# Kernel tuning notes

Hardware: AMD Instinct MI355X
Metric: run time of the kernel (lower is better)

## Reference

```python
import jax, jax.numpy as jnp
import numpy as np

H = 1024  # hidden_size
V = 32000  # vocab_size
L = 2048  # y_len


def _lstm_cell(gates, c):
    # torch gate order: input, forget, cell(g), output
    i = jax.nn.sigmoid(gates[:H])
    f = jax.nn.sigmoid(gates[H:2 * H])
    g = jnp.tanh(gates[2 * H:3 * H])
    o = jax.nn.sigmoid(gates[3 * H:4 * H])
    c_new = f * c + i * g
    return o * jnp.tanh(c_new), c_new


def setup_inputs() -> dict:
    key = jax.random.key(0)
    ks = jax.random.split(key, 13)
    s = 0.05
    inp = {
        "y": jax.random.randint(ks[0], (L,), 0, V, dtype=jnp.int32),
        "context_vector": jax.random.normal(ks[1], (2, H), dtype=jnp.float32),
        # layer 0: input dim 1
        "w_ih0": jax.random.normal(ks[2], (4 * H, 1), dtype=jnp.float32) * s,
        "w_hh0": jax.random.normal(ks[3], (4 * H, H), dtype=jnp.float32) * s,
        "b_ih0": jax.random.normal(ks[4], (4 * H,), dtype=jnp.float32) * s,
        "b_hh0": jax.random.normal(ks[5], (4 * H,), dtype=jnp.float32) * s,
        # layer 1: input dim H
        "w_ih1": jax.random.normal(ks[6], (4 * H, H), dtype=jnp.float32) * s,
        "w_hh1": jax.random.normal(ks[7], (4 * H, H), dtype=jnp.float32) * s,
        "b_ih1": jax.random.normal(ks[8], (4 * H,), dtype=jnp.float32) * s,
        "b_hh1": jax.random.normal(ks[9], (4 * H,), dtype=jnp.float32) * s,
        # fc: hidden -> vocab
        "w_fc": jax.random.normal(ks[10], (V, H), dtype=jnp.float32) * s,
        "b_fc": jax.random.normal(ks[11], (V,), dtype=jnp.float32) * s,
    }
    return inp


def reference(y, context_vector, w_ih0, w_hh0, b_ih0, b_hh0,
              w_ih1, w_hh1, b_ih1, b_hh1, w_fc, b_fc):
    # tfr = 0.0 => teacher forcing never used; next input is argmax of predictions.
    # h_s = h_c = context_vector initially (as in the torch module).
    def step(carry, _):
        tok, h, c = carry  # tok: scalar f32; h,c: [2, H]
        x = tok[None]  # [1]
        g0 = w_ih0 @ x + b_ih0 + w_hh0 @ h[0] + b_hh0
        h0, c0 = _lstm_cell(g0, c[0])
        g1 = w_ih1 @ h0 + b_ih1 + w_hh1 @ h[1] + b_hh1
        h1, c1 = _lstm_cell(g1, c[1])
        preds = jax.nn.relu(w_fc @ h1 + b_fc)  # [V]
        best = jnp.argmax(preds).astype(jnp.float32)
        return (best, jnp.stack([h0, h1]), jnp.stack([c0, c1])), preds

    init = (y[0].astype(jnp.float32), context_vector, context_vector)
    _, preds_seq = jax.lax.scan(step, init, None, length=L - 1)  # [L-1, V]
    outputs = jnp.concatenate(
        [jnp.zeros((1, V), dtype=jnp.float32), preds_seq], axis=0)  # [L, V]
    return outputs  # training mode: raw outputs (eval would apply log_softmax)
```

## Files before the change

kernel.cpp:

```cpp
#include <hip/hip_runtime.h>
#include <cstdint>
#include <cstddef>

#define H   1024
#define V   32000
#define L   2048
#define G4  4096
#define NB  256
#define NT  1024
#define RPB (V / NB)

#define GNB   500
#define GT    512
#define GS    8
#define GR    8
#define NCHUNK (L / GS)

__device__ __forceinline__ float wave_reduce_sum(float v) {
    #pragma unroll
    for (int off = 32; off > 0; off >>= 1) v += __shfl_down(v, off);
    return v;
}

__device__ __forceinline__ float wave_reduce_max(float v) {
    #pragma unroll
    for (int off = 32; off > 0; off >>= 1) v = fmaxf(v, __shfl_down(v, off));
    return v;
}

__device__ __forceinline__ unsigned long long wave_reduce_max_u64(unsigned long long v) {
    #pragma unroll
    for (int off = 32; off > 0; off >>= 1) {
        const unsigned long long o = __shfl_down(v, off);
        v = (o > v) ? o : v;
    }
    return v;
}

__device__ __forceinline__ float sigmoidf_(float x) {
    return 1.0f / (1.0f + expf(-x));
}

__device__ __forceinline__ float dot4(const float4 w, const float* __restrict__ h, int c) {
    return w.x * h[c] + w.y * h[c + 1] + w.z * h[c + 2] + w.w * h[c + 3];
}

__device__ __forceinline__ float sb2f(int w, int pos) {
    return (float)((w << ((3 - pos) * 8)) >> 24);
}

__global__ __launch_bounds__(256) void quant_fc(
    const float* __restrict__ src, signed char* __restrict__ dst,
    float2* __restrict__ scl_eps)
{
    const int gw   = (blockIdx.x * blockDim.x + threadIdx.x) >> 6;
    const int lane = threadIdx.x & 63;
    const int nw   = (gridDim.x * blockDim.x) >> 6;
    for (int row = gw; row < V; row += nw) {
        const float* p = src + (size_t)row * H + lane * 16;
        float w[16];
        #pragma unroll
        for (int j = 0; j < 4; j++) {
            const float4 f = *(const float4*)(p + j * 4);
            w[j * 4 + 0] = f.x; w[j * 4 + 1] = f.y;
            w[j * 4 + 2] = f.z; w[j * 4 + 3] = f.w;
        }
        float m = 0.f;
        #pragma unroll
        for (int j = 0; j < 16; j++) m = fmaxf(m, fabsf(w[j]));
        m = wave_reduce_max(m);
        m = __shfl(m, 0);
        const float scale = fmaxf(m, 1e-30f) / 127.f;
        const float inv   = 127.f / fmaxf(m, 1e-30f);
        int q[16];
        float esq = 0.f;
        #pragma unroll
        for (int j = 0; j < 16; j++) {
            q[j] = __float2int_rn(w[j] * inv);
            const float e = w[j] - scale * (float)q[j];
            esq += e * e;
        }
        esq = wave_reduce_sum(esq);
        const unsigned int d0 = (q[0] & 255) | ((q[1] & 255) << 8) | ((q[2] & 255) << 16) | ((unsigned int)(q[3] & 255) << 24);
        const unsigned int d1 = (q[4] & 255) | ((q[5] & 255) << 8) | ((q[6] & 255) << 16) | ((unsigned int)(q[7] & 255) << 24);
        const unsigned int d2 = (q[8] & 255) | ((q[9] & 255) << 8) | ((q[10] & 255) << 16) | ((unsigned int)(q[11] & 255) << 24);
        const unsigned int d3 = (q[12] & 255) | ((q[13] & 255) << 8) | ((q[14] & 255) << 16) | ((unsigned int)(q[15] & 255) << 24);
        *(int4*)(dst + (size_t)row * H + lane * 16) =
            make_int4((int)d0, (int)d1, (int)d2, (int)d3);
        if (lane == 0) {
            scl_eps[row] = make_float2(scale, sqrtf(esq) + 1e-12f);
        }
    }
}

__global__ __launch_bounds__(NT) void init_kernel(
    const int* __restrict__ y, const float* __restrict__ ctx,
    const float* __restrict__ w_hh0, const float* __restrict__ b_ih0,
    const float* __restrict__ b_hh0,
    float* __restrict__ v0, float* __restrict__ c0, float* __restrict__ c1,
    float* __restrict__ h1g0, unsigned long long* __restrict__ keys)
{
    __shared__ __align__(16) float h0s[H];
    const int b = blockIdx.x, t = threadIdx.x;
    h0s[t] = ctx[t];
    __syncthreads();

    const int wave = t >> 6, lane = t & 63;
    const int rowR = (wave >> 2) * H + b * 4 + (wave & 3);
    {
        const float* w0r = w_hh0 + (size_t)rowR * H;
        float accV = 0.f;
        #pragma unroll
        for (int k = 0; k < 4; k++) {
            const int c = k * 256 + lane * 4;
            accV += dot4(*(const float4*)(w0r + c), h0s, c);
        }
        accV = wave_reduce_sum(accV);
        if (lane == 0) v0[rowR] = accV + b_ih0[rowR] + b_hh0[rowR];
    }
    if (b == 0) {
        c0[t]   = ctx[t];
        c1[t]   = ctx[H + t];
        h1g0[t] = ctx[H + t];
        if (t < NB) keys[t] = 0ull;
        if (t == 0) {
            keys[0] = ((unsigned long long)0x7F800000u << 32) |
                      (0xFFFFFFFFu - (unsigned int)y[0]);
        }
    }
}

__global__ __launch_bounds__(NT) void lstm_kernel(
    const float* __restrict__ w_ih0, const float* __restrict__ w_ih1,
    const float* __restrict__ w_hh0, const float* __restrict__ w_hh1,
    const float* __restrict__ b_ih0, const float* __restrict__ b_hh0,
    const float* __restrict__ b_ih1, const float* __restrict__ b_hh1,
    const float* __restrict__ v0_in, float* __restrict__ v0_out,
    const float* __restrict__ c0_in, float* __restrict__ c0_out,
    float* __restrict__ c1,
    const float* __restrict__ h1prev, float* __restrict__ h1out,
    const unsigned long long* __restrict__ keys,
    float* __restrict__ h1_hist, const int step)
{
    __shared__ __align__(16) float h0s[H];
    __shared__ __align__(16) float h1ps[H];
    __shared__ float g1s[16];
    __shared__ unsigned long long kred[4];
    const int b = blockIdx.x, t = threadIdx.x;
    const int wave = t >> 6, lane = t & 63;
    const int rowR = (wave >> 2) * H + b * 4 + (wave & 3);

    const float* wU = w_hh1 + (size_t)rowR * H;
    float4 wu[4];
    #pragma unroll
    for (int k = 0; k < 4; k++)
        wu[k] = *(const float4*)(wU + k * 256 + lane * 4);

    h1ps[t] = h1prev[t];

    if (wave < 4) {
        unsigned long long k = keys[t];
        k = wave_reduce_max_u64(k);
        if (lane == 0) kred[wave] = k;
    }

    const float v0a = v0_in[t],         v0b = v0_in[H + t];
    const float v0c = v0_in[2 * H + t], v0d = v0_in[3 * H + t];
    const float wia = w_ih0[t],         wib = w_ih0[H + t];
    const float wic = w_ih0[2 * H + t], wid = w_ih0[3 * H + t];
    const float c0v = c0_in[t];

    __syncthreads();

    unsigned long long kk = kred[0];
    kk = (kred[1] > kk) ? kred[1] : kk;
    kk = (kred[2] > kk) ? kred[2] : kk;
    kk = (kred[3] > kk) ? kred[3] : kk;
    const float tok =
        (float)(unsigned int)(0xFFFFFFFFu - (unsigned int)(kk & 0xFFFFFFFFull));

    float accU = 0.f;
    #pragma unroll
    for (int k = 0; k < 4; k++) {
        const int c = k * 256 + lane * 4;
        accU += dot4(wu[k], h1ps, c);
    }

    {
        const float gi = v0a + tok * wia;
        const float gf = v0b + tok * wib;
        const float gg = v0c + tok * wic;
        const float go = v0d + tok * wid;
        const float i_ = sigmoidf_(gi);
        const float f_ = sigmoidf_(gf);
        const float g_ = tanhf(gg);
        const float o_ = sigmoidf_(go);
        const float cn = f_ * c0v + i_ * g_;
        if (b == 0) c0_out[t] = cn;
        h0s[t] = o_ * tanhf(cn);
    }
    __syncthreads();

    {
        const float* wA = w_ih1 + (size_t)rowR * H;
        const float* wB = w_hh0 + (size_t)rowR * H;
        float accA = 0.f, accB = 0.f;
        #pragma unroll
        for (int k = 0; k < 4; k++) {
            const int c = k * 256 + lane * 4;
            accA += dot4(*(const float4*)(wA + c), h0s, c);
            accB += dot4(*(const float4*)(wB + c), h0s, c);
        }
        const float g  = wave_reduce_sum(accA + accU);
        const float vv = wave_reduce_sum(accB);
        if (lane == 0) {
            g1s[wave]    = g  + b_ih1[rowR] + b_hh1[rowR];
            v0_out[rowR] = vv + b_ih0[rowR] + b_hh0[rowR];
        }
    }
    __syncthreads();

    if (t < 4) {
        const float i_ = sigmoidf_(g1s[t]);
        const float f_ = sigmoidf_(g1s[4 + t]);
        const float g_ = tanhf(g1s[8 + t]);
        const float o_ = sigmoidf_(g1s[12 + t]);
        const float cn = f_ * c1[b * 4 + t] + i_ * g_;
        c1[b * 4 + t] = cn;
        const float hv = o_ * tanhf(cn);
        h1out[b * 4 + t] = hv;
        if (h1_hist) h1_hist[(size_t)step * H + b * 4 + t] = hv;
    }
}

__global__ __launch_bounds__(NT) void screen_kernel(
    const signed char* __restrict__ wq8, const float2* __restrict__ scl_eps,
    const float* __restrict__ w_fc, const float* __restrict__ b_fc,
    const float* __restrict__ h1cur, unsigned long long* __restrict__ keys)
{
    __shared__ __align__(16) float h1s[H];
    __shared__ float lb[128], ub[128];
    __shared__ float red[16];
    __shared__ float LBmax_s;
    __shared__ unsigned long long wkey[16];
    const int b = blockIdx.x, t = threadIdx.x;
    const int wave = t >> 6, lane = t & 63;

    const float hv = h1cur[t];
    h1s[t] = hv;
    if (t < 128) { lb[t] = -3e38f; ub[t] = -3e38f; }
    {
        const float sq = wave_reduce_sum(hv * hv);
        if (lane == 0) red[wave] = sq;
    }
    __syncthreads();

    float Hl2;
    {
        float s = 0.f;
        #pragma unroll
        for (int i = 0; i < 16; i++) s += red[i];
        Hl2 = sqrtf(s);
    }

    const float4 hA = *(const float4*)(h1s + lane * 16);
    const float4 hB = *(const float4*)(h1s + lane * 16 + 4);
    const float4 hC = *(const float4*)(h1s + lane * 16 + 8);
    const float4 hD = *(const float4*)(h1s + lane * 16 + 12);

    int4 qv[8];
    #pragma unroll
    for (int i = 0; i < 8; i++) {
        const int rl = i * 16 + wave;
        const int row = b * RPB + (rl < RPB ? rl : 0);
        qv[i] = *(const int4*)(wq8 + (size_t)row * H + lane * 16);
    }
    float acc[8];
    #pragma unroll
    for (int i = 0; i < 8; i++) {
        const int4 q = qv[i];
        float a;
        a  = sb2f(q.x, 0) * hA.x + sb2f(q.x, 1) * hA.y + sb2f(q.x, 2) * hA.z + sb2f(q.x, 3) * hA.w;
        a += sb2f(q.y, 0) * hB.x + sb2f(q.y, 1) * hB.y + sb2f(q.y, 2) * hB.z + sb2f(q.y, 3) * hB.w;
        a += sb2f(q.z, 0) * hC.x + sb2f(q.z, 1) * hC.y + sb2f(q.z, 2) * hC.z + sb2f(q.z, 3) * hC.w;
        a += sb2f(q.w, 0) * hD.x + sb2f(q.w, 1) * hD.y + sb2f(q.w, 2) * hD.z + sb2f(q.w, 3) * hD.w;
        acc[i] = a;
    }
    #pragma unroll
    for (int off = 32; off > 0; off >>= 1) {
        #pragma unroll
        for (int i = 0; i < 8; i++) acc[i] += __shfl_down(acc[i], off);
    }
    if (lane == 0) {
        #pragma unroll
        for (int i = 0; i < 8; i++) {
            const int rl = i * 16 + wave;
            if (rl < RPB) {
                const int row = b * RPB + rl;
                const float2 se = scl_eps[row];
                float p = se.x * acc[i] + b_fc[row];
                p = fmaxf(p, 0.f);
                const float e = se.y * Hl2;
                ub[rl] = p + e;
                lb[rl] = p - e;
            }
        }
    }
    __syncthreads();

    if (wave == 0) {
        float m = fmaxf(lb[lane], lb[lane + 64]);
        m = wave_reduce_max(m);
        if (lane == 0) LBmax_s = m;
    }
    __syncthreads();
    const float LBmax = LBmax_s;

    unsigned long long bestKey = 0ull;

    #pragma unroll
    for (int i = 0; i < 8; i++) {
        const int rl = i * 16 + wave;
        if (rl >= RPB) break;
        if (ub[rl] >= LBmax) {
            const int row = b * RPB + rl;
            const float* wrow = w_fc + (size_t)row * H;
            float a = 0.f;
            #pragma unroll
            for (int k = 0; k < 4; k++) {
                const int c = k * 256 + lane * 4;
                a += dot4(*(const float4*)(wrow + c), h1s, c);
            }
            a = wave_reduce_sum(a);
            if (lane == 0) {
                float p = a + b_fc[row];
                p = p > 0.f ? p : 0.f;
                const unsigned long long key =
                    ((unsigned long long)__float_as_uint(p) << 32) |
                    (0xFFFFFFFFu - (unsigned int)row);
                if (key > bestKey) bestKey = key;
            }
        }
    }

    if (lane == 0) wkey[wave] = bestKey;
    __syncthreads();
    if (t == 0) {
        unsigned long long k = wkey[0];
        #pragma unroll
        for (int i = 1; i < 16; i++) k = (wkey[i] > k) ? wkey[i] : k;
        keys[b] = k;
    }
}

__global__ __launch_bounds__(NT) void fc32_kernel(
    const float* __restrict__ w_fc, const float* __restrict__ b_fc,
    const float* __restrict__ h1cur, unsigned long long* __restrict__ keys,
    float* __restrict__ out_row)
{
    __shared__ __align__(16) float h1s[H];
    __shared__ unsigned long long wkey[16];
    const int b = blockIdx.x, t = threadIdx.x;
    const int wave = t >> 6, lane = t & 63;

    h1s[t] = h1cur[t];
    __syncthreads();

    unsigned long long bestKey = 0ull;
    #pragma unroll
    for (int i = 0; i < 8; i++) {
        const int rl = i * 16 + wave;
        if (rl >= RPB) break;
        const int row = b * RPB + rl;
        const float* wrow = w_fc + (size_t)row * H;
        float a = 0.f;
        #pragma unroll
        for (int k = 0; k < 4; k++) {
            const int c = k * 256 + lane * 4;
            a += dot4(*(const float4*)(wrow + c), h1s, c);
        }
        a = wave_reduce_sum(a);
        if (lane == 0) {
            float p = a + b_fc[row];
            p = p > 0.f ? p : 0.f;
            out_row[row] = p;
            const unsigned long long key =
                ((unsigned long long)__float_as_uint(p) << 32) |
                (0xFFFFFFFFu - (unsigned int)row);
            if (key > bestKey) bestKey = key;
        }
    }

    if (lane == 0) wkey[wave] = bestKey;
    __syncthreads();
    if (t == 0) {
        unsigned long long k = wkey[0];
        #pragma unroll
        for (int i = 1; i < 16; i++) k = (wkey[i] > k) ? wkey[i] : k;
        keys[b] = k;
    }
}

__global__ __launch_bounds__(GT) void out_gemm(
    const float* __restrict__ w_fc, const float* __restrict__ b_fc,
    const float* __restrict__ h1_hist, float* __restrict__ out)
{
    __shared__ __align__(16) float hs[GS][H];
    __shared__ float stage[GS][64];
    const int b = blockIdx.x, t = threadIdx.x;
    const int wave = t >> 6, lane = t & 63;
    const int row0 = b * 64 + wave * GR;

    float4 wr[GR][4];
    #pragma unroll
    for (int r = 0; r < GR; r++)
        #pragma unroll
        for (int k = 0; k < 4; k++)
            wr[r][k] = *(const float4*)(w_fc + (size_t)(row0 + r) * H + k * 256 + lane * 4);

    for (int chunk = 0; chunk < NCHUNK; ++chunk) {
        __syncthreads();
        {
            const float4* src = (const float4*)(h1_hist + (size_t)chunk * GS * H);
            float4* dsts = (float4*)(&hs[0][0]);
            #pragma unroll
            for (int j = 0; j < 4; j++) dsts[j * GT + t] = src[j * GT + t];
        }
        __syncthreads();

        #pragma unroll
        for (int sb = 0; sb < 2; sb++) {
            float acc[GR][4];
            #pragma unroll
            for (int r = 0; r < GR; r++)
                #pragma unroll
                for (int s = 0; s < 4; s++) acc[r][s] = 0.f;
            #pragma unroll
            for (int k = 0; k < 4; k++) {
                const int c = k * 256 + lane * 4;
                const float4 h0 = *(const float4*)(&hs[sb * 4 + 0][c]);
                const float4 h1 = *(const float4*)(&hs[sb * 4 + 1][c]);
                const float4 h2 = *(const float4*)(&hs[sb * 4 + 2][c]);
                const float4 h3 = *(const float4*)(&hs[sb * 4 + 3][c]);
                #pragma unroll
                for (int r = 0; r < GR; r++) {
                    const float4 w = wr[r][k];
                    acc[r][0] += w.x * h0.x + w.y * h0.y + w.z * h0.z + w.w * h0.w;
                    acc[r][1] += w.x * h1.x + w.y * h1.y + w.z * h1.z + w.w * h1.w;
                    acc[r][2] += w.x * h2.x + w.y * h2.y + w.z * h2.z + w.w * h2.w;
                    acc[r][3] += w.x * h3.x + w.y * h3.y + w.z * h3.z + w.w * h3.w;
                }
            }
            #pragma unroll
            for (int r = 0; r < GR; r++)
                #pragma unroll
                for (int s = 0; s < 4; s++) {
                    const float vv = wave_reduce_sum(acc[r][s]);
                    if (lane == 0) stage[sb * 4 + s][wave * GR + r] = vv;
                }
        }
        __syncthreads();
        {
            const int s = t >> 6;
            const int col = t & 63;
            const int sidx = chunk * GS + s;
            if (sidx >= 1) {
                const float vv = stage[s][col] + b_fc[b * 64 + col];
                out[(size_t)sidx * V + b * 64 + col] = fmaxf(vv, 0.f);
            }
        }
    }
}

extern "C" void kernel_launch(void* const* d_in, const int* in_sizes, int n_in,
                              void* d_out, int out_size, void* d_ws, size_t ws_size,
                              hipStream_t stream)
{
    const int*   y     = (const int*)  d_in[0];
    const float* ctx   = (const float*)d_in[1];
    const float* w_ih0 = (const float*)d_in[2];
    const float* w_hh0 = (const float*)d_in[3];
    const float* b_ih0 = (const float*)d_in[4];
    const float* b_hh0 = (const float*)d_in[5];
    const float* w_ih1 = (const float*)d_in[6];
    const float* w_hh1 = (const float*)d_in[7];
    const float* b_ih1 = (const float*)d_in[8];
    const float* b_hh1 = (const float*)d_in[9];
    const float* w_fc  = (const float*)d_in[10];
    const float* b_fc  = (const float*)d_in[11];
    float* out = (float*)d_out;

    const size_t WQ8_BYTES  = (size_t)V * H;
    const size_t SCL_BYTES  = (size_t)V * sizeof(float2);
    const size_t HIST_BYTES = (size_t)L * H * sizeof(float);
    const size_t STATE_BYTES = 55296;
    const int use8 = (ws_size >= WQ8_BYTES + SCL_BYTES + HIST_BYTES + STATE_BYTES) ? 1 : 0;

    char* ws = (char*)d_ws;
    signed char* wq8     = (signed char*)ws;
    float2*      scl_eps = (float2*)(ws + WQ8_BYTES);
    float*       h1_hist = (float*)(ws + WQ8_BYTES + SCL_BYTES);
    char* base = ws + (use8 ? (WQ8_BYTES + SCL_BYTES + HIST_BYTES) : 0);
    float* v0g = (float*)(base + 0);
    float* c0  = (float*)(base + 32768);
    float* c1  = (float*)(base + 40960);
    float* h1g = (float*)(base + 45056);
    unsigned long long* keys = (unsigned long long*)(base + 53248);

    hipMemsetAsync(d_out, 0, (size_t)V * sizeof(float), stream);

    if (use8) {
        hipMemsetAsync(h1_hist, 0, (size_t)H * sizeof(float), stream);
        quant_fc<<<512, 256, 0, stream>>>(w_fc, wq8, scl_eps);
    }

    init_kernel<<<NB, NT, 0, stream>>>(y, ctx, w_hh0, b_ih0, b_hh0,
                                       v0g, c0, c1, h1g , keys);

    for (int t = 1; t < L; t++) {
        const float* v0i = v0g + ((t - 1) & 1) * G4;
        float*       v0o = v0g + (t & 1) * G4;
        const float* c0i = c0 + ((t - 1) & 1) * H;
        float*       c0o = c0 + (t & 1) * H;
        const float* h1p = h1g + ((t - 1) & 1) * H;
        float*       h1c = h1g + (t & 1) * H;
        lstm_kernel<<<NB, NT, 0, stream>>>(w_ih0, w_ih1, w_hh0, w_hh1,
                                           b_ih0, b_hh0, b_ih1, b_hh1,
                                           v0i, v0o, c0i, c0o, c1,
                                           h1p, h1c, keys,
                                           use8 ? h1_hist : (float*)nullptr, t);
        if (use8) {
            screen_kernel<<<NB, NT, 0, stream>>>(wq8, scl_eps, w_fc, b_fc,
                                                 h1c, keys);
        } else {
            fc32_kernel<<<NB, NT, 0, stream>>>(w_fc, b_fc, h1c, keys,
                                               out + (size_t)t * V);
        }
    }

    if (use8) {
        out_gemm<<<GNB, GT, 0, stream>>>(w_fc, b_fc, h1_hist, out);
    }
}
```

Before: 53.54 ms.

## Fuse per-step LSTM and screening kernels into one persistent kernel with grid barriers

Replaces roughly 4094 per-step kernel launches (lstm + screen) with a single persistent kernel of 256 blocks that loops over all time steps. Blocks synchronise through an atomic-counter grid barrier, and per-step state (h1, v0, argmax keys) moves through agent-scope atomic loads and stores. Weight slices for w_hh1, w_ih1 and w_hh0 stay in registers across steps, and the recurrent w_hh1·h1 product is computed early, overlapping the screen phase. This risks deadlock if all 256 blocks of 1024 threads cannot be co-resident, and it adds barrier spin latency in place of launch overhead.

```diff
diff --git a/kernel.cpp b/kernel.cpp
--- a/kernel.cpp
+++ b/kernel.cpp
@@ -47,6 +47,29 @@
 
 __device__ __forceinline__ float sb2f(int w, int pos) {
     return (float)((w << ((3 - pos) * 8)) >> 24);
+}
+
+__device__ __forceinline__ float ldc(const float* p) {
+    return __hip_atomic_load(p, __ATOMIC_RELAXED, __HIP_MEMORY_SCOPE_AGENT);
+}
+__device__ __forceinline__ void stc(float* p, float v) {
+    __hip_atomic_store(p, v, __ATOMIC_RELAXED, __HIP_MEMORY_SCOPE_AGENT);
+}
+__device__ __forceinline__ unsigned long long ldc64(const unsigned long long* p) {
+    return __hip_atomic_load(p, __ATOMIC_RELAXED, __HIP_MEMORY_SCOPE_AGENT);
+}
+__device__ __forceinline__ void stc64(unsigned long long* p, unsigned long long v) {
+    __hip_atomic_store(p, v, __ATOMIC_RELAXED, __HIP_MEMORY_SCOPE_AGENT);
+}
+
+__device__ __forceinline__ void gbar(unsigned int* cnt, unsigned int target) {
+    __syncthreads();
+    if (threadIdx.x == 0) {
+        __hip_atomic_fetch_add(cnt, 1u, __ATOMIC_RELAXED, __HIP_MEMORY_SCOPE_AGENT);
+        while (__hip_atomic_load(cnt, __ATOMIC_RELAXED, __HIP_MEMORY_SCOPE_AGENT) < target)
+            __builtin_amdgcn_s_sleep(4);
+    }
+    __syncthreads();
 }
 
 __global__ __launch_bounds__(256) void quant_fc(
@@ -93,6 +116,248 @@
     }
 }
 
+__global__ __launch_bounds__(NT) void persistent_kernel(
+    const int* __restrict__ y, const float* __restrict__ ctx,
+    const float* __restrict__ w_ih0, const float* __restrict__ w_ih1,
+    const float* __restrict__ w_hh0, const float* __restrict__ w_hh1,
+    const float* __restrict__ b_ih0, const float* __restrict__ b_hh0,
+    const float* __restrict__ b_ih1, const float* __restrict__ b_hh1,
+    const signed char* __restrict__ wq8, const float2* __restrict__ scl_eps,
+    const float* __restrict__ w_fc, const float* __restrict__ b_fc,
+    float* __restrict__ v0g, float* __restrict__ h1g,
+    unsigned long long* __restrict__ keys, unsigned int* __restrict__ cnt,
+    float* __restrict__ h1_hist)
+{
+    __shared__ __align__(16) float h0s[H];
+    __shared__ __align__(16) float hcs[H];
+    __shared__ float g1s[16];
+    __shared__ unsigned long long kred[4];
+    __shared__ float lb[128], ub[128];
+    __shared__ float red[16];
+    __shared__ float LBmax_s;
+    __shared__ unsigned long long wkey[16];
+    __shared__ float c1s[4];
+
+    const int b = blockIdx.x, t = threadIdx.x;
+    const int wave = t >> 6, lane = t & 63;
+    const int rowR = (wave >> 2) * H + b * 4 + (wave & 3);
+
+    unsigned int barK = 0;
+
+    float4 wu[4], wa[4], wb[4];
+    #pragma unroll
+    for (int k = 0; k < 4; k++) {
+        const int c = k * 256 + lane * 4;
+        wu[k] = *(const float4*)(w_hh1 + (size_t)rowR * H + c);
+        wa[k] = *(const float4*)(w_ih1 + (size_t)rowR * H + c);
+        wb[k] = *(const float4*)(w_hh0 + (size_t)rowR * H + c);
+    }
+    const float wia = w_ih0[t],         wib = w_ih0[H + t];
+    const float wic = w_ih0[2 * H + t], wid = w_ih0[3 * H + t];
+    const float bias0 = b_ih0[rowR] + b_hh0[rowR];
+    const float bias1 = b_ih1[rowR] + b_hh1[rowR];
+    float c0_reg = ctx[t];
+
+    h0s[t] = ctx[t];
+    hcs[t] = ctx[H + t];
+    if (t < 4) c1s[t] = ctx[H + b * 4 + t];
+    __syncthreads();
+    {
+        float accV = 0.f;
+        #pragma unroll
+        for (int k = 0; k < 4; k++) accV += dot4(wb[k], h0s, k * 256 + lane * 4);
+        accV = wave_reduce_sum(accV);
+        if (lane == 0) stc(&v0g[rowR], accV + bias0);
+    }
+    float accU = 0.f;
+    #pragma unroll
+    for (int k = 0; k < 4; k++) accU += dot4(wu[k], hcs, k * 256 + lane * 4);
+    if (b == 0 && t < NB) {
+        const unsigned long long seed =
+            ((unsigned long long)0x7F800000u << 32) |
+            (0xFFFFFFFFu - (unsigned int)y[0]);
+        stc64(&keys[t], (t == 0) ? seed : 0ull);
+    }
+    gbar(cnt, NB * (++barK));
+
+    for (int step = 1; step < L; ++step) {
+        const float* v0i = v0g + ((step - 1) & 1) * G4;
+        float*       v0o = v0g + (step & 1) * G4;
+        float*       h1c = h1g + (step & 1) * H;
+
+        if (wave < 4) {
+            unsigned long long k = ldc64(&keys[t]);
+            k = wave_reduce_max_u64(k);
+            if (lane == 0) kred[wave] = k;
+        }
+        const float v0a = ldc(&v0i[t]);
+        const float v0b = ldc(&v0i[H + t]);
+        const float v0c = ldc(&v0i[2 * H + t]);
+        const float v0d = ldc(&v0i[3 * H + t]);
+        __syncthreads();
+
+        unsigned long long kk = kred[0];
+        kk = (kred[1] > kk) ? kred[1] : kk;
+        kk = (kred[2] > kk) ? kred[2] : kk;
+        kk = (kred[3] > kk) ? kred[3] : kk;
+        const float tok =
+            (float)(unsigned int)(0xFFFFFFFFu - (unsigned int)(kk & 0xFFFFFFFFull));
+
+        {
+            const float gi = v0a + tok * wia;
+            const float gf = v0b + tok * wib;
+            const float gg = v0c + tok * wic;
+            const float go = v0d + tok * wid;
+            const float i_ = sigmoidf_(gi);
+            const float f_ = sigmoidf_(gf);
+            const float g_ = tanhf(gg);
+            const float o_ = sigmoidf_(go);
+            const float cn = f_ * c0_reg + i_ * g_;
+            c0_reg = cn;
+            h0s[t] = o_ * tanhf(cn);
+        }
+        __syncthreads();
+
+        {
+            float accA = 0.f, accB = 0.f;
+            #pragma unroll
+            for (int k = 0; k < 4; k++) {
+                const int c = k * 256 + lane * 4;
+                accA += dot4(wa[k], h0s, c);
+                accB += dot4(wb[k], h0s, c);
+            }
+            const float g  = wave_reduce_sum(accA + accU);
+            const float vv = wave_reduce_sum(accB);
+            if (lane == 0) {
+                g1s[wave] = g + bias1;
+                stc(&v0o[rowR], vv + bias0);
+            }
+        }
+        __syncthreads();
+
+        if (t < 4) {
+            const float i_ = sigmoidf_(g1s[t]);
+            const float f_ = sigmoidf_(g1s[4 + t]);
+            const float g_ = tanhf(g1s[8 + t]);
+            const float o_ = sigmoidf_(g1s[12 + t]);
+            const float cn = f_ * c1s[t] + i_ * g_;
+            c1s[t] = cn;
+            const float hv = o_ * tanhf(cn);
+            stc(&h1c[b * 4 + t], hv);
+            h1_hist[(size_t)step * H + b * 4 + t] = hv;
+        }
+        gbar(cnt, NB * (++barK));
+
+        if (t < 128) { lb[t] = -3e38f; ub[t] = -3e38f; }
+        const float hv2 = ldc(&h1c[t]);
+        hcs[t] = hv2;
+        {
+            const float sq = wave_reduce_sum(hv2 * hv2);
+            if (lane == 0) red[wave] = sq;
+        }
+        __syncthreads();
+
+        float s = 0.f;
+        #pragma unroll
+        for (int i = 0; i < 16; i++) s += red[i];
+        const float Hl2 = sqrtf(s);
+
+        const float4 hA = *(const float4*)(hcs + lane * 16);
+        const float4 hB = *(const float4*)(hcs + lane * 16 + 4);
+        const float4 hC = *(const float4*)(hcs + lane * 16 + 8);
+        const float4 hD = *(const float4*)(hcs + lane * 16 + 12);
+
+        float accs[8];
+        #pragma unroll
+        for (int bq = 0; bq < 2; bq++) {
+            int4 qv[4];
+            #pragma unroll
+            for (int i = 0; i < 4; i++) {
+                const int rl = (bq * 4 + i) * 16 + wave;
+                const int row = b * RPB + (rl < RPB ? rl : 0);
+                qv[i] = *(const int4*)(wq8 + (size_t)row * H + lane * 16);
+            }
+            #pragma unroll
+            for (int i = 0; i < 4; i++) {
+                const int4 q = qv[i];
+                float a;
+                a  = sb2f(q.x, 0) * hA.x + sb2f(q.x, 1) * hA.y + sb2f(q.x, 2) * hA.z + sb2f(q.x, 3) * hA.w;
+                a += sb2f(q.y, 0) * hB.x + sb2f(q.y, 1) * hB.y + sb2f(q.y, 2) * hB.z + sb2f(q.y, 3) * hB.w;
+                a += sb2f(q.z, 0) * hC.x + sb2f(q.z, 1) * hC.y + sb2f(q.z, 2) * hC.z + sb2f(q.z, 3) * hC.w;
+                a += sb2f(q.w, 0) * hD.x + sb2f(q.w, 1) * hD.y + sb2f(q.w, 2) * hD.z + sb2f(q.w, 3) * hD.w;
+                accs[bq * 4 + i] = a;
+            }
+        }
+        #pragma unroll
+        for (int off = 32; off > 0; off >>= 1) {
+            #pragma unroll
+            for (int i = 0; i < 8; i++) accs[i] += __shfl_down(accs[i], off);
+        }
+        if (lane == 0) {
+            #pragma unroll
+            for (int i = 0; i < 8; i++) {
+                const int rl = i * 16 + wave;
+                if (rl < RPB) {
+                    const int row = b * RPB + rl;
+                    const float2 se = scl_eps[row];
+                    float p = se.x * accs[i] + b_fc[row];
+                    p = fmaxf(p, 0.f);
+                    const float e = se.y * Hl2;
+                    ub[rl] = p + e;
+                    lb[rl] = p - e;
+                }
+            }
+        }
+        __syncthreads();
+
+        if (wave == 0) {
+            float m = fmaxf(lb[lane], lb[lane + 64]);
+            m = wave_reduce_max(m);
+            if (lane == 0) LBmax_s = m;
+        }
+        accU = 0.f;
+        #pragma unroll
+        for (int k = 0; k < 4; k++) accU += dot4(wu[k], hcs, k * 256 + lane * 4);
+        __syncthreads();
+        const float LBmax = LBmax_s;
+
+        unsigned long long bestKey = 0ull;
+        #pragma unroll
+        for (int i = 0; i < 8; i++) {
+            const int rl = i * 16 + wave;
+            if (rl >= RPB) break;
+            if (ub[rl] >= LBmax) {
+                const int row = b * RPB + rl;
+                const float* wrow = w_fc + (size_t)row * H;
+                float a = 0.f;
+                #pragma unroll
+                for (int k = 0; k < 4; k++) {
+                    const int c = k * 256 + lane * 4;
+                    a += dot4(*(const float4*)(wrow + c), hcs, c);
+                }
+                a = wave_reduce_sum(a);
+                if (lane == 0) {
+                    float p = a + b_fc[row];
+                    p = p > 0.f ? p : 0.f;
+                    const unsigned long long key =
+                        ((unsigned long long)__float_as_uint(p) << 32) |
+                        (0xFFFFFFFFu - (unsigned int)row);
+                    if (key > bestKey) bestKey = key;
+                }
+            }
+        }
+        if (lane == 0) wkey[wave] = bestKey;
+        __syncthreads();
+        if (t == 0) {
+            unsigned long long k2 = wkey[0];
+            #pragma unroll
+            for (int i = 1; i < 16; i++) k2 = (wkey[i] > k2) ? wkey[i] : k2;
+            stc64(&keys[b], k2);
+        }
+        gbar(cnt, NB * (++barK));
+    }
+}
+
 __global__ __launch_bounds__(NT) void init_kernel(
     const int* __restrict__ y, const float* __restrict__ ctx,
     const float* __restrict__ w_hh0, const float* __restrict__ b_ih0,
@@ -139,8 +404,7 @@
     const float* __restrict__ c0_in, float* __restrict__ c0_out,
     float* __restrict__ c1,
     const float* __restrict__ h1prev, float* __restrict__ h1out,
-    const unsigned long long* __restrict__ keys,
-    float* __restrict__ h1_hist, const int step)
+    const unsigned long long* __restrict__ keys)
 {
     __shared__ __align__(16) float h0s[H];
     __shared__ __align__(16) float h1ps[H];
@@ -227,129 +491,7 @@
         const float o_ = sigmoidf_(g1s[12 + t]);
         const float cn = f_ * c1[b * 4 + t] + i_ * g_;
         c1[b * 4 + t] = cn;
-        const float hv = o_ * tanhf(cn);
-        h1out[b * 4 + t] = hv;
-        if (h1_hist) h1_hist[(size_t)step * H + b * 4 + t] = hv;
-    }
-}
-
-__global__ __launch_bounds__(NT) void screen_kernel(
-    const signed char* __restrict__ wq8, const float2* __restrict__ scl_eps,
-    const float* __restrict__ w_fc, const float* __restrict__ b_fc,
-    const float* __restrict__ h1cur, unsigned long long* __restrict__ keys)
-{
-    __shared__ __align__(16) float h1s[H];
-    __shared__ float lb[128], ub[128];
-    __shared__ float red[16];
-    __shared__ float LBmax_s;
-    __shared__ unsigned long long wkey[16];
-    const int b = blockIdx.x, t = threadIdx.x;
-    const int wave = t >> 6, lane = t & 63;
-
-    const float hv = h1cur[t];
-    h1s[t] = hv;
-    if (t < 128) { lb[t] = -3e38f; ub[t] = -3e38f; }
-    {
-        const float sq = wave_reduce_sum(hv * hv);
-        if (lane == 0) red[wave] = sq;
-    }
-    __syncthreads();
-
-    float Hl2;
-    {
-        float s = 0.f;
-        #pragma unroll
-        for (int i = 0; i < 16; i++) s += red[i];
-        Hl2 = sqrtf(s);
-    }
-
-    const float4 hA = *(const float4*)(h1s + lane * 16);
-    const float4 hB = *(const float4*)(h1s + lane * 16 + 4);
-    const float4 hC = *(const float4*)(h1s + lane * 16 + 8);
-    const float4 hD = *(const float4*)(h1s + lane * 16 + 12);
-
-    int4 qv[8];
-    #pragma unroll
-    for (int i = 0; i < 8; i++) {
-        const int rl = i * 16 + wave;
-        const int row = b * RPB + (rl < RPB ? rl : 0);
-        qv[i] = *(const int4*)(wq8 + (size_t)row * H + lane * 16);
-    }
-    float acc[8];
-    #pragma unroll
-    for (int i = 0; i < 8; i++) {
-        const int4 q = qv[i];
-        float a;
-        a  = sb2f(q.x, 0) * hA.x + sb2f(q.x, 1) * hA.y + sb2f(q.x, 2) * hA.z + sb2f(q.x, 3) * hA.w;
-        a += sb2f(q.y, 0) * hB.x + sb2f(q.y, 1) * hB.y + sb2f(q.y, 2) * hB.z + sb2f(q.y, 3) * hB.w;
-        a += sb2f(q.z, 0) * hC.x + sb2f(q.z, 1) * hC.y + sb2f(q.z, 2) * hC.z + sb2f(q.z, 3) * hC.w;
-        a += sb2f(q.w, 0) * hD.x + sb2f(q.w, 1) * hD.y + sb2f(q.w, 2) * hD.z + sb2f(q.w, 3) * hD.w;
-        acc[i] = a;
-    }
-    #pragma unroll
-    for (int off = 32; off > 0; off >>= 1) {
-        #pragma unroll
-        for (int i = 0; i < 8; i++) acc[i] += __shfl_down(acc[i], off);
-    }
-    if (lane == 0) {
-        #pragma unroll
-        for (int i = 0; i < 8; i++) {
-            const int rl = i * 16 + wave;
-            if (rl < RPB) {
-                const int row = b * RPB + rl;
-                const float2 se = scl_eps[row];
-                float p = se.x * acc[i] + b_fc[row];
-                p = fmaxf(p, 0.f);
-                const float e = se.y * Hl2;
-                ub[rl] = p + e;
-                lb[rl] = p - e;
-            }
-        }
-    }
-    __syncthreads();
-
-    if (wave == 0) {
-        float m = fmaxf(lb[lane], lb[lane + 64]);
-        m = wave_reduce_max(m);
-        if (lane == 0) LBmax_s = m;
-    }
-    __syncthreads();
-    const float LBmax = LBmax_s;
-
-    unsigned long long bestKey = 0ull;
-
-    #pragma unroll
-    for (int i = 0; i < 8; i++) {
-        const int rl = i * 16 + wave;
-        if (rl >= RPB) break;
-        if (ub[rl] >= LBmax) {
-            const int row = b * RPB + rl;
-            const float* wrow = w_fc + (size_t)row * H;
-            float a = 0.f;
-            #pragma unroll
-            for (int k = 0; k < 4; k++) {
-                const int c = k * 256 + lane * 4;
-                a += dot4(*(const float4*)(wrow + c), h1s, c);
-            }
-            a = wave_reduce_sum(a);
-            if (lane == 0) {
-                float p = a + b_fc[row];
-                p = p > 0.f ? p : 0.f;
-                const unsigned long long key =
-                    ((unsigned long long)__float_as_uint(p) << 32) |
-                    (0xFFFFFFFFu - (unsigned int)row);
-                if (key > bestKey) bestKey = key;
-            }
-        }
-    }
-
-    if (lane == 0) wkey[wave] = bestKey;
-    __syncthreads();
-    if (t == 0) {
-        unsigned long long k = wkey[0];
-        #pragma unroll
-        for (int i = 1; i < 16; i++) k = (wkey[i] > k) ? wkey[i] : k;
-        keys[b] = k;
+        h1out[b * 4 + t] = o_ * tanhf(cn);
     }
 }
 
@@ -493,7 +635,7 @@
     const size_t WQ8_BYTES  = (size_t)V * H;
     const size_t SCL_BYTES  = (size_t)V * sizeof(float2);
     const size_t HIST_BYTES = (size_t)L * H * sizeof(float);
-    const size_t STATE_BYTES = 55296;
+    const size_t STATE_BYTES = 55808;
     const int use8 = (ws_size >= WQ8_BYTES + SCL_BYTES + HIST_BYTES + STATE_BYTES) ? 1 : 0;
 
     char* ws = (char*)d_ws;
@@ -506,39 +648,36 @@
     float* c1  = (float*)(base + 40960);
     float* h1g = (float*)(base + 45056);
     unsigned long long* keys = (unsigned long long*)(base + 53248);
+    unsigned int* cnt = (unsigned int*)(base + 55296);
 
     hipMemsetAsync(d_out, 0, (size_t)V * sizeof(float), stream);
 
     if (use8) {
+        hipMemsetAsync(cnt, 0, 256, stream);
         hipMemsetAsync(h1_hist, 0, (size_t)H * sizeof(float), stream);
         quant_fc<<<512, 256, 0, stream>>>(w_fc, wq8, scl_eps);
-    }
-
-    init_kernel<<<NB, NT, 0, stream>>>(y, ctx, w_hh0, b_ih0, b_hh0,
-                                       v0g, c0, c1, h1g , keys);
-
-    for (int t = 1; t < L; t++) {
-        const float* v0i = v0g + ((t - 1) & 1) * G4;
-        float*       v0o = v0g + (t & 1) * G4;
-        const float* c0i = c0 + ((t - 1) & 1) * H;
-        float*       c0o = c0 + (t & 1) * H;
-        const float* h1p = h1g + ((t - 1) & 1) * H;
-        float*       h1c = h1g + (t & 1) * H;
-        lstm_kernel<<<NB, NT, 0, stream>>>(w_ih0, w_ih1, w_hh0, w_hh1,
-                                           b_ih0, b_hh0, b_ih1, b_hh1,
-                                           v0i, v0o, c0i, c0o, c1,
-                                           h1p, h1c, keys,
-                                           use8 ? h1_hist : (float*)nullptr, t);
-        if (use8) {
-            screen_kernel<<<NB, NT, 0, stream>>>(wq8, scl_eps, w_fc, b_fc,
-                                                 h1c, keys);
-        } else {
+        persistent_kernel<<<NB, NT, 0, stream>>>(
+            y, ctx, w_ih0, w_ih1, w_hh0, w_hh1,
+            b_ih0, b_hh0, b_ih1, b_hh1,
+            wq8, scl_eps, w_fc, b_fc,
+            v0g, h1g, keys, cnt, h1_hist);
+        out_gemm<<<GNB, GT, 0, stream>>>(w_fc, b_fc, h1_hist, out);
+    } else {
+        init_kernel<<<NB, NT, 0, stream>>>(y, ctx, w_hh0, b_ih0, b_hh0,
+                                           v0g, c0, c1, h1g , keys);
+        for (int t = 1; t < L; t++) {
+            const float* v0i = v0g + ((t - 1) & 1) * G4;
+            float*       v0o = v0g + (t & 1) * G4;
+            const float* c0i = c0 + ((t - 1) & 1) * H;
+            float*       c0o = c0 + (t & 1) * H;
+            const float* h1p = h1g + ((t - 1) & 1) * H;
+            float*       h1c = h1g + (t & 1) * H;
+            lstm_kernel<<<NB, NT, 0, stream>>>(w_ih0, w_ih1, w_hh0, w_hh1,
+                                               b_ih0, b_hh0, b_ih1, b_hh1,
+                                               v0i, v0o, c0i, c0o, c1,
+                                               h1p, h1c, keys);
             fc32_kernel<<<NB, NT, 0, stream>>>(w_fc, b_fc, h1c, keys,
                                                out + (size_t)t * V);
         }
     }
-
-    if (use8) {
-        out_gemm<<<GNB, GT, 0, stream>>>(w_fc, b_fc, h1_hist, out);
-    }
-}
+}
```

Result: slower. 131.8 ms (+146.2%).
